# Optimization experiments

Measured on AMD Instinct MI355X. Metric: run time of the kernel, lower is better.

## Reference

```python
import jax, jax.numpy as jnp
import numpy as np
import math

B, C, H, W, K, HID = 8, 64, 512, 512, 8, 64

def setup_inputs() -> dict:
    key = jax.random.key(0)
    ks = jax.random.split(key, 12)
    s = 0.05  # weight scale
    return {
        "x": jax.random.normal(ks[0], (B, C, H, W), dtype=jnp.float32),
        "w1k": jax.random.normal(ks[1], (1, HID), dtype=jnp.float32) * s,
        "b1k": jax.random.normal(ks[2], (HID,), dtype=jnp.float32) * s,
        "w2k": jax.random.normal(ks[3], (HID, K * K), dtype=jnp.float32) * s,
        "b2k": jax.random.normal(ks[4], (K * K,), dtype=jnp.float32) * s,
        "w1b": jax.random.normal(ks[5], (1, HID), dtype=jnp.float32) * s,
        "b1b": jax.random.normal(ks[6], (HID,), dtype=jnp.float32) * s,
        "w2b": jax.random.normal(ks[7], (HID, 1), dtype=jnp.float32) * s,
        "b2b": jax.random.normal(ks[8], (1,), dtype=jnp.float32) * s,
        "conv_w": jax.random.normal(ks[9], (C, C), dtype=jnp.float32) * s,
        "conv_b": jax.random.normal(ks[10], (C,), dtype=jnp.float32) * s,
    }

def _patch_pos_dist(h, w, k):
    # normalized distance of each KxK patch center from the image center, row-major over (nh, nw)
    nh, nw = h // k, w // k
    cy, cx = h / 2.0, w / 2.0
    max_d = math.sqrt(cy ** 2 + cx ** 2)
    py = jnp.arange(nh, dtype=jnp.float32) * k + k / 2.0
    px = jnp.arange(nw, dtype=jnp.float32) * k + k / 2.0
    d = jnp.sqrt((py - cy)[:, None] ** 2 + (px - cx)[None, :] ** 2) / max_d
    return d.reshape(nh * nw)  # [L]

def reference(x, w1k, b1k, w2k, b2k, w1b, b1b, w2b, b2b, conv_w, conv_b):
    b, c, h, w = x.shape
    kk = w2k.shape[1]
    k = int(round(math.sqrt(kk)))
    nh, nw = h // k, w // k
    L = nh * nw

    d = _patch_pos_dist(h, w, k)[:, None]  # [L, 1]
    # dynamic per-patch-position kernels and bias (exact-erf GELU as in torch default)
    pk = jax.nn.gelu(d @ w1k + b1k, approximate=False) @ w2k + b2k          # [L, K*K]
    pb = (jax.nn.gelu(d @ w1b + b1b, approximate=False) @ w2b + b2b)[:, 0]  # [L]

    # non-overlapping unfold: [B, C, K*K, L], patches row-major over (nh, nw)
    patches = (x.reshape(b, c, nh, k, nw, k)
                 .transpose(0, 1, 2, 4, 3, 5)
                 .reshape(b, c, L, kk)
                 .transpose(0, 1, 3, 2))

    feats = jnp.einsum('bckl,lk->bcl', patches, pk) + pb[None, None, :]     # [B, C, L]
    feats = jnp.einsum('oc,bcl->bol', conv_w, feats) + conv_b[None, :, None]  # 1x1 conv

    mod = patches * feats[:, :, None, :]  # [B, C, K*K, L]

    # fold back (non-overlapping, so a pure reshape/scatter)
    out = (mod.transpose(0, 1, 3, 2)
              .reshape(b, c, nh, nw, k, k)
              .transpose(0, 1, 2, 4, 3, 5)
              .reshape(b, c, h, w))
    return out
```

## Files before the change

### kernel.cpp

```cpp
#include <hip/hip_runtime.h>
#include <math.h>


static __device__ __forceinline__ float gelu_erf(float x) {
    return 0.5f * x * (1.0f + erff(x * 0.70710678118654752f));
}

__global__ __launch_bounds__(256) void mlp_precompute(
    const float* __restrict__ w1k, const float* __restrict__ b1k,
    const float* __restrict__ w2k, const float* __restrict__ b2k,
    const float* __restrict__ w1b, const float* __restrict__ b1b,
    const float* __restrict__ w2b, const float* __restrict__ b2b,
    float* __restrict__ pk_out,
    float* __restrict__ pb_out)
{
    constexpr int HID = 64;
    const int tid = threadIdx.x;
    const int pi  = tid >> 6;
    const int j   = tid & 63;
    const int l   = blockIdx.x * 4 + pi;

    const int py_i = l >> 6;
    const int px_i = l & 63;
    const float py = (float)(py_i * 8) + 4.0f - 256.0f;
    const float px = (float)(px_i * 8) + 4.0f - 256.0f;
    const float dd = sqrtf(py * py + px * px) * (1.0f / 362.03867196751236f);

    __shared__ float gk[4][HID];
    __shared__ float gb[4][HID];

    gk[pi][j] = gelu_erf(dd * w1k[j] + b1k[j]);
    gb[pi][j] = gelu_erf(dd * w1b[j] + b1b[j]);
    __syncthreads();

    float s = b2k[j];
#pragma unroll 8
    for (int h = 0; h < HID; ++h)
        s += gk[pi][h] * w2k[h * HID + j];
    pk_out[l * HID + j] = s;

    if (j == 0) {
        float t = b2b[0];
        for (int h = 0; h < HID; ++h)
            t += gb[pi][h] * w2b[h];
        pb_out[l] = t;
    }
}

__global__ __launch_bounds__(512, 4) void afpm_main(
    const float* __restrict__ x,
    const float* __restrict__ conv_w, const float* __restrict__ conv_b,
    const float* __restrict__ pk_g,
    const float* __restrict__ pb_g,
    float* __restrict__ out)
{
    constexpr int W = 512;

    const int tid = threadIdx.x;
    const int q   = tid & 1;
    const int pw  = (tid >> 1) & 3;
    const int c   = tid >> 3;
    const int pwg = blockIdx.x;
    const int ph  = blockIdx.y;
    const int b   = blockIdx.z;

    __shared__ float convT[64 * 65];
    __shared__ float f0T[4][68];

    const int l = ph * 64 + pwg * 4 + pw;

    const size_t cbase = (((size_t)b * 64 + c) * 512 + (size_t)ph * 8) * (size_t)W
                         + (size_t)(pwg * 32 + pw * 8 + q * 4);
    const float* xp = x + cbase;
    float4 v[8];
#pragma unroll
    for (int r = 0; r < 8; ++r)
        v[r] = *(const float4*)(xp + r * W);

    const float4* pkp = (const float4*)pk_g + (size_t)l * 16 + q;
    float4 kv[8];
#pragma unroll
    for (int r = 0; r < 8; ++r)
        kv[r] = pkp[r * 2];

    const float pbv = pb_g[l];
    const float cbv = conv_b[c];

    {
        const float4* cw4 = (const float4*)conv_w;
        const float4 w0 = cw4[tid * 2 + 0];
        const float4 w1 = cw4[tid * 2 + 1];
        const int o   = tid >> 3;
        const int cc0 = (tid & 7) * 8;
        convT[(cc0 + 0) * 65 + o] = w0.x; convT[(cc0 + 1) * 65 + o] = w0.y;
        convT[(cc0 + 2) * 65 + o] = w0.z; convT[(cc0 + 3) * 65 + o] = w0.w;
        convT[(cc0 + 4) * 65 + o] = w1.x; convT[(cc0 + 5) * 65 + o] = w1.y;
        convT[(cc0 + 6) * 65 + o] = w1.z; convT[(cc0 + 7) * 65 + o] = w1.w;
    }

    float s = 0.0f;
#pragma unroll
    for (int r = 0; r < 8; ++r) {
        s += v[r].x * kv[r].x + v[r].y * kv[r].y
           + v[r].z * kv[r].z + v[r].w * kv[r].w;
    }
    s += __shfl_xor(s, 1);
    if (q == 0)
        f0T[pw][c] = s + pbv;

    __syncthreads();

    const float* f0p = &f0T[pw][q * 32];
    float t = 0.0f;
#pragma unroll
    for (int i4 = 0; i4 < 8; ++i4) {
        const float4 f = *(const float4*)(f0p + i4 * 4);
        const int ccb = q * 32 + i4 * 4;
        t += convT[(ccb + 0) * 65 + c] * f.x
           + convT[(ccb + 1) * 65 + c] * f.y
           + convT[(ccb + 2) * 65 + c] * f.z
           + convT[(ccb + 3) * 65 + c] * f.w;
    }
    t += __shfl_xor(t, 1);
    const float m = t + cbv;

    float* op = out + cbase;
#pragma unroll
    for (int r = 0; r < 8; ++r) {
        float4 a = v[r];
        a.x *= m; a.y *= m; a.z *= m; a.w *= m;
        *(float4*)(op + r * W) = a;
    }
}

extern "C" void kernel_launch(void* const* d_in, const int* in_sizes, int n_in,
                              void* d_out, int out_size, void* d_ws, size_t ws_size,
                              hipStream_t stream) {
    const float* x      = (const float*)d_in[0];
    const float* w1k    = (const float*)d_in[1];
    const float* b1k    = (const float*)d_in[2];
    const float* w2k    = (const float*)d_in[3];
    const float* b2k    = (const float*)d_in[4];
    const float* w1b    = (const float*)d_in[5];
    const float* b1b    = (const float*)d_in[6];
    const float* w2b    = (const float*)d_in[7];
    const float* b2b    = (const float*)d_in[8];
    const float* conv_w = (const float*)d_in[9];
    const float* conv_b = (const float*)d_in[10];
    float* out = (float*)d_out;

    constexpr int L = 64 * 64;
    float* pk = (float*)d_ws;
    float* pb = pk + (size_t)L * 64;

    mlp_precompute<<<L / 4, 256, 0, stream>>>(w1k, b1k, w2k, b2k,
                                              w1b, b1b, w2b, b2b, pk, pb);

    dim3 grid(16, 64, 8);
    afpm_main<<<grid, 512, 0, stream>>>(x, conv_w, conv_b, pk, pb, out);
}
```

Baseline: 234.6 us.

## Drop shared conv weight transpose, read conv_w directly and raise occupancy

Removes the per-block shared-memory transpose of the 64x64 conv weight and instead reads each output channel's weight row straight from global memory as float4s, which should stay cached. The pk vector loads move into the dot-product loop, and the pb/conv_b loads are deferred, to cut register pressure. Launch bounds are raised to request 8 blocks of 512 threads per CU. This lowers LDS use and register count so more blocks can be resident to hide the memory-bound load latency, at the cost of more global or cache traffic for the conv weights and later-issued loads.

```diff
diff --git a/kernel.cpp b/kernel.cpp
--- a/kernel.cpp
+++ b/kernel.cpp
@@ -47,7 +47,7 @@
     }
 }
 
-__global__ __launch_bounds__(512, 4) void afpm_main(
+__global__ __launch_bounds__(512, 8) void afpm_main(
     const float* __restrict__ x,
     const float* __restrict__ conv_w, const float* __restrict__ conv_b,
     const float* __restrict__ pk_g,
@@ -64,7 +64,6 @@
     const int ph  = blockIdx.y;
     const int b   = blockIdx.z;
 
-    __shared__ float convT[64 * 65];
     __shared__ float f0T[4][68];
 
     const int l = ph * 64 + pwg * 4 + pw;
@@ -78,51 +77,29 @@
         v[r] = *(const float4*)(xp + r * W);
 
     const float4* pkp = (const float4*)pk_g + (size_t)l * 16 + q;
-    float4 kv[8];
-#pragma unroll
-    for (int r = 0; r < 8; ++r)
-        kv[r] = pkp[r * 2];
-
-    const float pbv = pb_g[l];
-    const float cbv = conv_b[c];
-
-    {
-        const float4* cw4 = (const float4*)conv_w;
-        const float4 w0 = cw4[tid * 2 + 0];
-        const float4 w1 = cw4[tid * 2 + 1];
-        const int o   = tid >> 3;
-        const int cc0 = (tid & 7) * 8;
-        convT[(cc0 + 0) * 65 + o] = w0.x; convT[(cc0 + 1) * 65 + o] = w0.y;
-        convT[(cc0 + 2) * 65 + o] = w0.z; convT[(cc0 + 3) * 65 + o] = w0.w;
-        convT[(cc0 + 4) * 65 + o] = w1.x; convT[(cc0 + 5) * 65 + o] = w1.y;
-        convT[(cc0 + 6) * 65 + o] = w1.z; convT[(cc0 + 7) * 65 + o] = w1.w;
-    }
-
     float s = 0.0f;
 #pragma unroll
     for (int r = 0; r < 8; ++r) {
-        s += v[r].x * kv[r].x + v[r].y * kv[r].y
-           + v[r].z * kv[r].z + v[r].w * kv[r].w;
+        const float4 kv = pkp[r * 2];
+        s += v[r].x * kv.x + v[r].y * kv.y + v[r].z * kv.z + v[r].w * kv.w;
     }
     s += __shfl_xor(s, 1);
     if (q == 0)
-        f0T[pw][c] = s + pbv;
+        f0T[pw][c] = s + pb_g[l];
 
     __syncthreads();
 
-    const float* f0p = &f0T[pw][q * 32];
+    const float4* cw  = (const float4*)(conv_w + (size_t)c * 64 + q * 32);
+    const float*  f0p = &f0T[pw][q * 32];
     float t = 0.0f;
 #pragma unroll
     for (int i4 = 0; i4 < 8; ++i4) {
+        const float4 w = cw[i4];
         const float4 f = *(const float4*)(f0p + i4 * 4);
-        const int ccb = q * 32 + i4 * 4;
-        t += convT[(ccb + 0) * 65 + c] * f.x
-           + convT[(ccb + 1) * 65 + c] * f.y
-           + convT[(ccb + 2) * 65 + c] * f.z
-           + convT[(ccb + 3) * 65 + c] * f.w;
+        t += w.x * f.x + w.y * f.y + w.z * f.z + w.w * f.w;
     }
     t += __shfl_xor(t, 1);
-    const float m = t + cbv;
+    const float m = t + conv_b[c];
 
     float* op = out + cbase;
 #pragma unroll
```

New measurement: 330.3 us. 1.41x slower.
